# Performance work log

Measured on AMD Instinct MI355X. Metric: run time of the kernel, lower is better.

The kernel has to match this reference:

```python
import jax, jax.numpy as jnp
import numpy as np

N_NODES = 100000
N_EDGES = 1600000
N_CLASS = 10
HIDDEN = 128
BN_EPS = 1e-5


def _bn(h, gamma, beta):
    # BatchNorm1d in training mode: biased batch statistics over the node dim
    m = h.mean(axis=0)
    v = ((h - m) ** 2).mean(axis=0)
    return gamma * (h - m) / jnp.sqrt(v + BN_EPS) + beta


def _mlp(h, w1, b1, g1, t1, w2, b2, g2, t2):
    h = jax.nn.relu(_bn(h @ w1 + b1, g1, t1))
    h = jax.nn.relu(_bn(h @ w2 + b2, g2, t2))
    return h


def _gin_conv(x, edge_index, mlp_params):
    src, dst = edge_index[0], edge_index[1]
    # sum-aggregate neighbor messages: [E, D] gather + scatter-add -> [N, D]
    agg = jax.ops.segment_sum(x[src], dst, num_segments=N_NODES)
    h = x + agg  # (1 + eps) * x + agg, eps = 0
    return _mlp(h, *mlp_params)


def setup_inputs() -> dict:
    key = jax.random.key(0)
    ks = jax.random.split(key, 16)
    x = jax.random.normal(ks[0], (N_NODES, N_CLASS), dtype=jnp.float32)
    edge_index = jax.random.randint(ks[1], (2, N_EDGES), 0, N_NODES, dtype=jnp.int64)
    edge_weight = jax.random.uniform(ks[2], (N_EDGES,), dtype=jnp.float32)

    def lin(k, fan_in, fan_out):
        bound = 1.0 / np.sqrt(fan_in)
        kw, kb = jax.random.split(k)
        w = jax.random.uniform(kw, (fan_in, fan_out), minval=-bound, maxval=bound, dtype=jnp.float32)
        b = jax.random.uniform(kb, (fan_out,), minval=-bound, maxval=bound, dtype=jnp.float32)
        return w, b

    w11, b11 = lin(ks[3], N_CLASS, HIDDEN)
    w12, b12 = lin(ks[4], HIDDEN, HIDDEN)
    w21, b21 = lin(ks[5], HIDDEN, HIDDEN)
    w22, b22 = lin(ks[6], HIDDEN, HIDDEN)
    wf, bf = lin(ks[7], HIDDEN, N_CLASS)
    ones = jnp.ones((HIDDEN,), jnp.float32)
    zeros = jnp.zeros((HIDDEN,), jnp.float32)
    return {
        "x": x, "edge_weight": edge_weight,
        "w11": w11, "b11": b11, "g11": ones, "t11": zeros,
        "w12": w12, "b12": b12, "g12": ones, "t12": zeros,
        "w21": w21, "b21": b21, "g21": ones, "t21": zeros,
        "w22": w22, "b22": b22, "g22": ones, "t22": zeros,
        "wf": wf, "bf": bf,
        "edge_index": edge_index,
    }


def reference(x, edge_weight, w11, b11, g11, t11, w12, b12, g12, t12,
              w21, b21, g21, t21, w22, b22, g22, t22, wf, bf, edge_index):
    h = jax.nn.relu(_gin_conv(x, edge_index, (w11, b11, g11, t11, w12, b12, g12, t12)))
    h = jax.nn.relu(_gin_conv(h, edge_index, (w21, b21, g21, t21, w22, b22, g22, t22)))
    logits = h @ wf + bf
    return jax.nn.log_softmax(logits, axis=1)
```

## Files before the change

### kernel.cpp

```cpp
#include <hip/hip_runtime.h>

#define N_CLASS 10
#define HIDDEN 128
#define BN_EPS 1e-5f

typedef short short8 __attribute__((ext_vector_type(8)));
typedef float floatx4 __attribute__((ext_vector_type(4)));

__device__ __forceinline__ float bf2f(unsigned short u) {
    unsigned int x = ((unsigned int)u) << 16;
    float f; __builtin_memcpy(&f, &x, 4); return f;
}
__device__ __forceinline__ unsigned short f2bf(float f) {
    unsigned int x; __builtin_memcpy(&x, &f, 4);
    x += 0x7FFFu + ((x >> 16) & 1u);
    return (unsigned short)(x >> 16);
}
__device__ __forceinline__ float lo_f(unsigned int u) {
    unsigned int x = u << 16; float f; __builtin_memcpy(&f, &x, 4); return f;
}
__device__ __forceinline__ float hi_f(unsigned int u) {
    unsigned int x = u & 0xffff0000u; float f; __builtin_memcpy(&f, &x, 4); return f;
}


__global__ __launch_bounds__(512) void bhist_k(const int* __restrict__ ei,
                                               int* __restrict__ bhist, int E) {
    __shared__ int h[512];
    int tid = threadIdx.x;
    h[tid] = 0;
    __syncthreads();
    for (int e = blockIdx.x * 512 + tid; e < E; e += gridDim.x * 512)
        atomicAdd(&h[((unsigned)ei[E + e]) >> 8], 1);
    __syncthreads();
    if (h[tid]) atomicAdd(&bhist[tid], h[tid]);
}

__global__ __launch_bounds__(512) void bscan_k(const int* __restrict__ bhist,
                                               int* __restrict__ bstart,
                                               int* __restrict__ bcur, int NBK) {
    __shared__ int sm[512];
    int t = threadIdx.x;
    sm[t] = (t < NBK) ? bhist[t] : 0;
    __syncthreads();
    for (int off = 1; off < 512; off <<= 1) {
        int u = (t >= off) ? sm[t - off] : 0;
        __syncthreads();
        sm[t] += u;
        __syncthreads();
    }
    int excl = (t == 0) ? 0 : sm[t - 1];
    if (t <= NBK) bstart[t] = excl;
    if (t < NBK)  bcur[t]   = excl;
}

__global__ __launch_bounds__(512) void bscatter_k(const int* __restrict__ ei,
                                                  int* __restrict__ bcur,
                                                  unsigned int* __restrict__ pairs, int E) {
    __shared__ int h[512], base[512], cur[512];
    int tid = threadIdx.x;
    h[tid] = 0; cur[tid] = 0;
    __syncthreads();
    int chunk = (E + gridDim.x - 1) / gridDim.x;
    int e0 = blockIdx.x * chunk;
    int e1 = min(e0 + chunk, E);
    for (int e = e0 + tid; e < e1; e += 512)
        atomicAdd(&h[((unsigned)ei[E + e]) >> 8], 1);
    __syncthreads();
    base[tid] = h[tid] ? atomicAdd(&bcur[tid], h[tid]) : 0;
    __syncthreads();
    for (int e = e0 + tid; e < e1; e += 512) {
        unsigned int s = (unsigned int)ei[e];
        unsigned int d = (unsigned int)ei[E + e];
        int bk = d >> 8;
        int r = atomicAdd(&cur[bk], 1);
        pairs[base[bk] + r] = s | ((d & 255u) << 24);
    }
}

__global__ __launch_bounds__(512) void bcsr_k(const unsigned int* __restrict__ pairs,
                                              const int* __restrict__ bstart,
                                              int* __restrict__ row_ptr,
                                              int* __restrict__ cnt,
                                              int* __restrict__ col, int N) {
    __shared__ int h[256], sc[256], cur[256];
    int tid = threadIdx.x;
    if (tid < 256) { h[tid] = 0; cur[tid] = 0; }
    __syncthreads();
    int b = blockIdx.x, lo = b << 8;
    int s = bstart[b], e = bstart[b + 1];
    for (int i = s + tid; i < e; i += 512)
        atomicAdd(&h[pairs[i] >> 24], 1);
    __syncthreads();
    if (tid < 256) sc[tid] = h[tid];
    __syncthreads();
    for (int off = 1; off < 256; off <<= 1) {
        int u = (tid < 256 && tid >= off) ? sc[tid - off] : 0;
        __syncthreads();
        if (tid < 256) sc[tid] += u;
        __syncthreads();
    }
    if (tid < 256) {
        int d = lo + tid;
        if (d < N) { cnt[d] = h[tid]; row_ptr[d] = s + sc[tid] - h[tid]; }
        sc[tid] -= h[tid];
    }
    __syncthreads();
    for (int i = s + tid; i < e; i += 512) {
        unsigned int p = pairs[i];
        int d = p >> 24;
        int r = atomicAdd(&cur[d], 1);
        col[s + sc[d] + r] = (int)(p & 0xFFFFFFu);
    }
}

__global__ void prep_k(const float* __restrict__ W0, const float* __restrict__ W1,
                       const float* __restrict__ W2,
                       unsigned short* __restrict__ T0, unsigned short* __restrict__ T1,
                       unsigned short* __restrict__ T2,
                       float* __restrict__ stats, int* __restrict__ bhist) {
    int y = blockIdx.y;
    int i = blockIdx.x * 256 + threadIdx.x;
    const float* W = (y == 0) ? W0 : (y == 1) ? W1 : W2;
    unsigned short* T = (y == 0) ? T0 : (y == 1) ? T1 : T2;
    if (i < 128 * 128) {
        int k = i >> 7, n = i & 127;
        T[n * 128 + k] = f2bf(W[k * 128 + n]);
    }
    if (y == 0) {
        if (i < 1024) stats[i] = 0.f;
        if (i < 512)  bhist[i] = 0;
    }
}

__global__ void padx_k(const float* __restrict__ X, unsigned short* __restrict__ XP, int N) {
    int i = blockIdx.x * 256 + threadIdx.x;
    if (i >= N * 16) return;
    int node = i >> 4, f = i & 15;
    XP[i] = (f < N_CLASS) ? f2bf(X[node * N_CLASS + f]) : (unsigned short)0;
}

__global__ void gather10_k(const unsigned short* __restrict__ XP, const int* __restrict__ col,
                           const int* __restrict__ rp, const int* __restrict__ cnt,
                           float* __restrict__ out, int N) {
    int t = blockIdx.x * 256 + threadIdx.x;
    int node = t >> 4, f = t & 15;
    if (node >= N) return;
    int start = rp[node], deg = cnt[node];
    float acc = bf2f(XP[node * 16 + f]);
    int j = 0;
    for (; j + 8 <= deg; j += 8) {
        int s0 = col[start + j],     s1 = col[start + j + 1];
        int s2 = col[start + j + 2], s3 = col[start + j + 3];
        int s4 = col[start + j + 4], s5 = col[start + j + 5];
        int s6 = col[start + j + 6], s7 = col[start + j + 7];
        float v0 = bf2f(XP[s0 * 16 + f]);
        float v1 = bf2f(XP[s1 * 16 + f]);
        float v2 = bf2f(XP[s2 * 16 + f]);
        float v3 = bf2f(XP[s3 * 16 + f]);
        float v4 = bf2f(XP[s4 * 16 + f]);
        float v5 = bf2f(XP[s5 * 16 + f]);
        float v6 = bf2f(XP[s6 * 16 + f]);
        float v7 = bf2f(XP[s7 * 16 + f]);
        acc += v0; acc += v1; acc += v2; acc += v3;
        acc += v4; acc += v5; acc += v6; acc += v7;
    }
    for (; j < deg; ++j)
        acc += bf2f(XP[col[start + j] * 16 + f]);
    out[node * 16 + f] = acc;
}

__global__ __launch_bounds__(256) void act2_k(
    const unsigned short* __restrict__ Z, unsigned short* __restrict__ R,
    const float* __restrict__ st, const float* __restrict__ g,
    const float* __restrict__ b, int N, float inv_n) {
    __shared__ float sTab[128], hTab[128];
    int tid = threadIdx.x;
    if (tid < 128) {
        float m = st[tid] * inv_n;
        float v = fmaxf(st[128 + tid] * inv_n - m * m, 0.f);
        float s = g[tid] * rsqrtf(v + BN_EPS);
        sTab[tid] = s;
        hTab[tid] = b[tid] - m * s;
    }
    __syncthreads();
    int total = N * 16;
    for (int i = blockIdx.x * 256 + tid; i < total; i += gridDim.x * 256) {
        int k8 = (i & 15) * 8;
        uint4 v = ((const uint4*)Z)[i];
        unsigned short* us = (unsigned short*)&v;
#pragma unroll
        for (int j = 0; j < 8; ++j) {
            float f = fmaxf(fmaf(bf2f(us[j]), sTab[k8 + j], hTab[k8 + j]), 0.f);
            us[j] = f2bf(f);
        }
        ((uint4*)R)[i] = v;
    }
}

__global__ __launch_bounds__(256) void gather_sum_k(
    const unsigned short* __restrict__ R, const int* __restrict__ col,
    const int* __restrict__ rp, const int* __restrict__ cnt,
    unsigned short* __restrict__ out, int N) {
    int wave = __builtin_amdgcn_readfirstlane((blockIdx.x * 256 + threadIdx.x) >> 6);
    int lane = threadIdx.x & 63;
    if (wave >= N) return;
    int start = __builtin_amdgcn_readfirstlane(rp[wave]);
    int deg   = __builtin_amdgcn_readfirstlane(cnt[wave]);
    const unsigned int* Xv = (const unsigned int*)R;
    unsigned int self = Xv[wave * 64 + lane];
    float a0 = lo_f(self);
    float a1 = hi_f(self);
    int j = 0;
    for (; j + 8 <= deg; j += 8) {
        int n0 = col[start + j],     n1 = col[start + j + 1];
        int n2 = col[start + j + 2], n3 = col[start + j + 3];
        int n4 = col[start + j + 4], n5 = col[start + j + 5];
        int n6 = col[start + j + 6], n7 = col[start + j + 7];
        unsigned int w0 = Xv[n0 * 64 + lane];
        unsigned int w1 = Xv[n1 * 64 + lane];
        unsigned int w2 = Xv[n2 * 64 + lane];
        unsigned int w3 = Xv[n3 * 64 + lane];
        unsigned int w4 = Xv[n4 * 64 + lane];
        unsigned int w5 = Xv[n5 * 64 + lane];
        unsigned int w6 = Xv[n6 * 64 + lane];
        unsigned int w7 = Xv[n7 * 64 + lane];
        a0 += lo_f(w0); a1 += hi_f(w0);
        a0 += lo_f(w1); a1 += hi_f(w1);
        a0 += lo_f(w2); a1 += hi_f(w2);
        a0 += lo_f(w3); a1 += hi_f(w3);
        a0 += lo_f(w4); a1 += hi_f(w4);
        a0 += lo_f(w5); a1 += hi_f(w5);
        a0 += lo_f(w6); a1 += hi_f(w6);
        a0 += lo_f(w7); a1 += hi_f(w7);
    }
    for (; j < deg; ++j) {
        unsigned int v = Xv[col[start + j] * 64 + lane];
        a0 += lo_f(v); a1 += hi_f(v);
    }
    unsigned int o = (unsigned int)f2bf(a0) | ((unsigned int)f2bf(a1) << 16);
    ((unsigned int*)out)[wave * 64 + lane] = o;
}

__global__ __launch_bounds__(128) void gemm10_k(
    const float* __restrict__ A, const float* __restrict__ W,
    const float* __restrict__ bias, unsigned short* __restrict__ C,
    float* __restrict__ stOut, int N) {
    __shared__ float rb[16 * 16];
    const int tid = threadIdx.x;
    float wreg[N_CLASS];
#pragma unroll
    for (int k = 0; k < N_CLASS; ++k) wreg[k] = W[k * HIDDEN + tid];
    float bb = bias[tid];
    float s = 0.f, s2 = 0.f;
    for (int r0 = blockIdx.x * 16; r0 < N; r0 += gridDim.x * 16) {
        int nr = min(16, N - r0);
        for (int i = tid; i < nr * 16; i += 128) rb[i] = A[r0 * 16 + i];
        __syncthreads();
        for (int r = 0; r < nr; ++r) {
            float acc = bb;
#pragma unroll
            for (int k = 0; k < N_CLASS; ++k) acc = fmaf(rb[r * 16 + k], wreg[k], acc);
            C[(r0 + r) * HIDDEN + tid] = f2bf(acc);
            s += acc; s2 += acc * acc;
        }
        __syncthreads();
    }
    atomicAdd(stOut + tid, s);
    atomicAdd(stOut + HIDDEN + tid, s2);
}

template<bool BN>
__global__ __launch_bounds__(256, 3) void gemm_mfma_k(
    const unsigned short* __restrict__ Zin, const unsigned short* __restrict__ Wt,
    const float* __restrict__ bias,
    const float* __restrict__ stIn, const float* __restrict__ gIn,
    const float* __restrict__ tIn,
    unsigned short* __restrict__ Zout, float* __restrict__ stOut,
    int N, float inv_n) {
    __shared__ unsigned short Wl[128 * 136];
    __shared__ unsigned short Al[64 * 136];
    __shared__ float sTab[128], hTab[128], biasTab[128];

    const int tid  = threadIdx.x;
    const int wv   = tid >> 6;
    const int ln   = tid & 63;
    const int half = ln >> 4;
    const int l16  = ln & 15;

    if (tid < 128) {
        biasTab[tid] = bias[tid];
        if (BN) {
            float m = stIn[tid] * inv_n;
            float v = fmaxf(stIn[128 + tid] * inv_n - m * m, 0.f);
            float s = gIn[tid] * rsqrtf(v + BN_EPS);
            sTab[tid] = s;
            hTab[tid] = tIn[tid] - m * s;
        }
    }
    for (int c = tid; c < 2048; c += 256) {
        int n = c >> 4, k8 = c & 15;
        uint4 v = *(const uint4*)(Wt + n * 128 + k8 * 8);
        *(uint4*)(&Wl[n * 136 + k8 * 8]) = v;
    }
    __syncthreads();

    float cs[8], cs2[8];
#pragma unroll
    for (int i = 0; i < 8; ++i) { cs[i] = 0.f; cs2[i] = 0.f; }

    const int ntiles = (N + 63) >> 6;
    for (int tile = blockIdx.x; tile < ntiles; tile += gridDim.x) {
        const int r0 = tile * 64;
        for (int c = tid; c < 1024; c += 256) {
            int r = c >> 4, k8 = c & 15;
            int gr = r0 + r; if (gr >= N) gr = N - 1;
            uint4 v = *(const uint4*)(Zin + gr * 128 + k8 * 8);
            if (BN) {
                unsigned short* us = (unsigned short*)&v;
                int kb = k8 * 8;
#pragma unroll
                for (int j = 0; j < 8; ++j) {
                    float f = fmaxf(fmaf(bf2f(us[j]), sTab[kb + j], hTab[kb + j]), 0.f);
                    us[j] = f2bf(f);
                }
            }
            *(uint4*)(&Al[r * 136 + k8 * 8]) = v;
        }
        __syncthreads();

        short8 afrag[4];
        const int arow = wv * 16 + l16;
#pragma unroll
        for (int s = 0; s < 4; ++s)
            afrag[s] = *(const short8*)(&Al[arow * 136 + s * 32 + half * 8]);
        __syncthreads();

#pragma unroll
        for (int ct = 0; ct < 8; ++ct) {
            floatx4 acc = {0.f, 0.f, 0.f, 0.f};
            const int bn_ = ct * 16 + l16;
#pragma unroll
            for (int s = 0; s < 4; ++s) {
                short8 bfrag = *(const short8*)(&Wl[bn_ * 136 + s * 32 + half * 8]);
                acc = __builtin_amdgcn_mfma_f32_16x16x32_bf16(afrag[s], bfrag, acc, 0, 0, 0);
            }
            float bcol = biasTab[bn_];
#pragma unroll
            for (int r = 0; r < 4; ++r) {
                int lrow = wv * 16 + half * 4 + r;
                float val = acc[r] + bcol;
                if (r0 + lrow < N) { cs[ct] += val; cs2[ct] += val * val; }
                Al[lrow * 136 + bn_] = f2bf(val);
            }
        }
        __syncthreads();

        for (int c = tid; c < 1024; c += 256) {
            int r = c >> 4, k8 = c & 15;
            int gr = r0 + r;
            if (gr < N)
                *(uint4*)(Zout + gr * 128 + k8 * 8) = *(const uint4*)(&Al[r * 136 + k8 * 8]);
        }
        __syncthreads();
    }

    float* red = (float*)Al;
    if (tid < 256) red[tid] = 0.f;
    __syncthreads();
#pragma unroll
    for (int ct = 0; ct < 8; ++ct) {
        float a = cs[ct], b = cs2[ct];
        a += __shfl_xor(a, 16); a += __shfl_xor(a, 32);
        b += __shfl_xor(b, 16); b += __shfl_xor(b, 32);
        if (half == 0) {
            atomicAdd(&red[ct * 16 + l16], a);
            atomicAdd(&red[128 + ct * 16 + l16], b);
        }
    }
    __syncthreads();
    if (tid < 128) {
        atomicAdd(stOut + tid, red[tid]);
        atomicAdd(stOut + 128 + tid, red[128 + tid]);
    }
}

__global__ __launch_bounds__(256) void final_mfma_k(
    const unsigned short* __restrict__ Z, const float* __restrict__ st,
    const float* __restrict__ g, const float* __restrict__ b,
    const float* __restrict__ wf, const float* __restrict__ bfc,
    float* __restrict__ out, int N, float inv_n) {
    __shared__ unsigned short Al[64 * 136];
    __shared__ unsigned short Bl[16 * 136];
    __shared__ float sTab[128], hTab[128], biasTab[16];

    const int tid  = threadIdx.x;
    const int wv   = tid >> 6;
    const int ln   = tid & 63;
    const int half = ln >> 4;
    const int l16  = ln & 15;

    if (tid < 128) {
        float m = st[tid] * inv_n;
        float v = fmaxf(st[128 + tid] * inv_n - m * m, 0.f);
        float s = g[tid] * rsqrtf(v + BN_EPS);
        sTab[tid] = s;
        hTab[tid] = b[tid] - m * s;
    }
    if (tid < 16) biasTab[tid] = (tid < N_CLASS) ? bfc[tid] : -3.0e38f;
    {
        int n = tid >> 4, k8 = (tid & 15) * 8;
        uint4 v;
        unsigned short* us = (unsigned short*)&v;
#pragma unroll
        for (int j = 0; j < 8; ++j)
            us[j] = (n < N_CLASS) ? f2bf(wf[(k8 + j) * N_CLASS + n]) : (unsigned short)0;
        *(uint4*)(&Bl[n * 136 + k8]) = v;
    }
    __syncthreads();

    short8 bfrag[4];
#pragma unroll
    for (int s = 0; s < 4; ++s)
        bfrag[s] = *(const short8*)(&Bl[l16 * 136 + s * 32 + half * 8]);

    const int ntiles = (N + 63) >> 6;
    for (int tile = blockIdx.x; tile < ntiles; tile += gridDim.x) {
        const int r0 = tile * 64;
        for (int c = tid; c < 1024; c += 256) {
            int r = c >> 4, k8 = c & 15;
            int gr = r0 + r; if (gr >= N) gr = N - 1;
            uint4 v = *(const uint4*)(Z + gr * 128 + k8 * 8);
            unsigned short* us = (unsigned short*)&v;
            int kb = k8 * 8;
#pragma unroll
            for (int j = 0; j < 8; ++j) {
                float f = fmaxf(fmaf(bf2f(us[j]), sTab[kb + j], hTab[kb + j]), 0.f);
                us[j] = f2bf(f);
            }
            *(uint4*)(&Al[r * 136 + k8 * 8]) = v;
        }
        __syncthreads();

        short8 afrag[4];
        const int arow = wv * 16 + l16;
#pragma unroll
        for (int s = 0; s < 4; ++s)
            afrag[s] = *(const short8*)(&Al[arow * 136 + s * 32 + half * 8]);
        __syncthreads();

        floatx4 acc = {0.f, 0.f, 0.f, 0.f};
#pragma unroll
        for (int s = 0; s < 4; ++s)
            acc = __builtin_amdgcn_mfma_f32_16x16x32_bf16(afrag[s], bfrag[s], acc, 0, 0, 0);

        float bcol = biasTab[l16];
#pragma unroll
        for (int r = 0; r < 4; ++r) {
            float lg = acc[r] + bcol;
            float mx = lg;
            mx = fmaxf(mx, __shfl_xor(mx, 1));
            mx = fmaxf(mx, __shfl_xor(mx, 2));
            mx = fmaxf(mx, __shfl_xor(mx, 4));
            mx = fmaxf(mx, __shfl_xor(mx, 8));
            float p = __expf(lg - mx);
            float se = p;
            se += __shfl_xor(se, 1);
            se += __shfl_xor(se, 2);
            se += __shfl_xor(se, 4);
            se += __shfl_xor(se, 8);
            float ls = __logf(se);
            int grow = r0 + wv * 16 + half * 4 + r;
            if (l16 < N_CLASS && grow < N)
                out[grow * N_CLASS + l16] = lg - mx - ls;
        }
    }
}


extern "C" void kernel_launch(void* const* d_in, const int* in_sizes, int n_in,
                              void* d_out, int out_size, void* d_ws, size_t ws_size,
                              hipStream_t stream) {
    const float* x   = (const float*)d_in[0];
    const float* w11 = (const float*)d_in[2];
    const float* b11 = (const float*)d_in[3];
    const float* g11 = (const float*)d_in[4];
    const float* t11 = (const float*)d_in[5];
    const float* w12 = (const float*)d_in[6];
    const float* b12 = (const float*)d_in[7];
    const float* g12 = (const float*)d_in[8];
    const float* t12 = (const float*)d_in[9];
    const float* w21 = (const float*)d_in[10];
    const float* b21 = (const float*)d_in[11];
    const float* g21 = (const float*)d_in[12];
    const float* t21 = (const float*)d_in[13];
    const float* w22 = (const float*)d_in[14];
    const float* b22 = (const float*)d_in[15];
    const float* g22 = (const float*)d_in[16];
    const float* t22 = (const float*)d_in[17];
    const float* wf  = (const float*)d_in[18];
    const float* bf  = (const float*)d_in[19];
    const int*   ei  = (const int*)d_in[20];

    const int N = in_sizes[0] / N_CLASS;
    const int E = in_sizes[1];
    const float inv_n = 1.0f / (float)N;
    const int NBK = (N + 255) >> 8;

    char* base = (char*)d_ws;
    size_t off = 0;
    auto take = [&](size_t bytes) { void* p = base + off; off += (bytes + 15) & ~(size_t)15; return p; };
    float*          stats   = (float*)take(1024 * 4);
    unsigned short* xp      = (unsigned short*)take((size_t)N * 16 * 2);
    float*          h0      = (float*)take((size_t)N * 16 * 4);
    int*            cnt     = (int*)take((size_t)N * 4);
    int*            row_ptr = (int*)take((size_t)N * 4);
    int*            bhist   = (int*)take(512 * 4);
    int*            bstart  = (int*)take(520 * 4);
    int*            bcur    = (int*)take(512 * 4);
    unsigned int*   pairs   = (unsigned int*)take((size_t)E * 4);
    int*            col     = (int*)take((size_t)E * 4);
    unsigned short* bufA    = (unsigned short*)take((size_t)N * HIDDEN * 2);
    unsigned short* bufB    = (unsigned short*)take((size_t)N * HIDDEN * 2);
    unsigned short* bufC    = (unsigned short*)take((size_t)N * HIDDEN * 2);
    unsigned short* Wt1     = (unsigned short*)take(128 * 128 * 2);
    unsigned short* Wt2     = (unsigned short*)take(128 * 128 * 2);
    unsigned short* Wt3     = (unsigned short*)take(128 * 128 * 2);

    prep_k<<<dim3(64, 3), 256, 0, stream>>>(w12, w21, w22, Wt1, Wt2, Wt3,
                                            stats, bhist);
    padx_k<<<(N * 16 + 255) / 256, 256, 0, stream>>>(x, xp, N);

    bhist_k<<<256, 512, 0, stream>>>(ei, bhist, E);
    bscan_k<<<1, 512, 0, stream>>>(bhist, bstart, bcur, NBK);
    bscatter_k<<<256, 512, 0, stream>>>(ei, bcur, pairs, E);
    bcsr_k<<<NBK, 512, 0, stream>>>(pairs, bstart, row_ptr, cnt, col, N);

    gather10_k<<<(N * 16 + 255) / 256, 256, 0, stream>>>(xp, col, row_ptr, cnt, h0, N);
    gemm10_k<<<512, 128, 0, stream>>>(h0, w11, b11, bufA, stats, N);
    gemm_mfma_k<true><<<768, 256, 0, stream>>>(bufA, Wt1, b12, stats, g11, t11,
                                               bufB, stats + 256, N, inv_n);

    act2_k<<<3125, 256, 0, stream>>>(bufB, bufC, stats + 256, g12, t12, N, inv_n);
    gather_sum_k<<<(N * 64 + 255) / 256, 256, 0, stream>>>(bufC, col, row_ptr, cnt,
                                                           bufA, N);

    gemm_mfma_k<false><<<768, 256, 0, stream>>>(bufA, Wt2, b21, nullptr, nullptr, nullptr,
                                                bufB, stats + 512, N, inv_n);
    gemm_mfma_k<true><<<768, 256, 0, stream>>>(bufB, Wt3, b22, stats + 512, g21, t21,
                                               bufA, stats + 768, N, inv_n);

    final_mfma_k<<<782, 256, 0, stream>>>(bufA, stats + 768, g22, t22,
                                          wf, bf, (float*)d_out, N, inv_n);
}
```

Measured before the change: 404.7 us.

## Precompute per-block bucket offsets via two-level scan; unroll gather by sixteen

The bucket sort now records a per-block histogram in bhist_k. A new bscan2_k kernel prefix-scans those counts into deterministic per-block base offsets, so bscatter_k no longer recounts its destination histogram or takes global atomic offsets. This removes one full pass over the destination indices and the atomic contention on bcur, at the cost of an extra small kernel launch and a 512x256 offset table. The hidden-layer gather loop also gets a 16-wide unrolled stage to keep more independent loads in flight per wave, which raises register pressure.

```diff
diff --git a/kernel.cpp b/kernel.cpp
--- a/kernel.cpp
+++ b/kernel.cpp
@@ -25,41 +25,11 @@
 
 
 __global__ __launch_bounds__(512) void bhist_k(const int* __restrict__ ei,
-                                               int* __restrict__ bhist, int E) {
+                                               int* __restrict__ bhist,
+                                               int* __restrict__ bbase, int E) {
     __shared__ int h[512];
     int tid = threadIdx.x;
     h[tid] = 0;
-    __syncthreads();
-    for (int e = blockIdx.x * 512 + tid; e < E; e += gridDim.x * 512)
-        atomicAdd(&h[((unsigned)ei[E + e]) >> 8], 1);
-    __syncthreads();
-    if (h[tid]) atomicAdd(&bhist[tid], h[tid]);
-}
-
-__global__ __launch_bounds__(512) void bscan_k(const int* __restrict__ bhist,
-                                               int* __restrict__ bstart,
-                                               int* __restrict__ bcur, int NBK) {
-    __shared__ int sm[512];
-    int t = threadIdx.x;
-    sm[t] = (t < NBK) ? bhist[t] : 0;
-    __syncthreads();
-    for (int off = 1; off < 512; off <<= 1) {
-        int u = (t >= off) ? sm[t - off] : 0;
-        __syncthreads();
-        sm[t] += u;
-        __syncthreads();
-    }
-    int excl = (t == 0) ? 0 : sm[t - 1];
-    if (t <= NBK) bstart[t] = excl;
-    if (t < NBK)  bcur[t]   = excl;
-}
-
-__global__ __launch_bounds__(512) void bscatter_k(const int* __restrict__ ei,
-                                                  int* __restrict__ bcur,
-                                                  unsigned int* __restrict__ pairs, int E) {
-    __shared__ int h[512], base[512], cur[512];
-    int tid = threadIdx.x;
-    h[tid] = 0; cur[tid] = 0;
     __syncthreads();
     int chunk = (E + gridDim.x - 1) / gridDim.x;
     int e0 = blockIdx.x * chunk;
@@ -67,8 +37,54 @@
     for (int e = e0 + tid; e < e1; e += 512)
         atomicAdd(&h[((unsigned)ei[E + e]) >> 8], 1);
     __syncthreads();
-    base[tid] = h[tid] ? atomicAdd(&bcur[tid], h[tid]) : 0;
-    __syncthreads();
+    bbase[tid * 256 + blockIdx.x] = h[tid];
+    if (h[tid]) atomicAdd(&bhist[tid], h[tid]);
+}
+
+__global__ __launch_bounds__(512) void bscan_k(const int* __restrict__ bhist,
+                                               int* __restrict__ bstart, int NBK) {
+    __shared__ int sm[512];
+    int t = threadIdx.x;
+    sm[t] = (t < NBK) ? bhist[t] : 0;
+    __syncthreads();
+    for (int off = 1; off < 512; off <<= 1) {
+        int u = (t >= off) ? sm[t - off] : 0;
+        __syncthreads();
+        sm[t] += u;
+        __syncthreads();
+    }
+    bstart[t] = (t == 0) ? 0 : sm[t - 1];
+    if (t == 0) bstart[512] = sm[511];
+}
+
+__global__ __launch_bounds__(256) void bscan2_k(int* __restrict__ bbase,
+                                                const int* __restrict__ bstart) {
+    __shared__ int sm[256];
+    int b = blockIdx.x;
+    int t = threadIdx.x;
+    int v = bbase[b * 256 + t];
+    sm[t] = v;
+    __syncthreads();
+    for (int off = 1; off < 256; off <<= 1) {
+        int u = (t >= off) ? sm[t - off] : 0;
+        __syncthreads();
+        sm[t] += u;
+        __syncthreads();
+    }
+    bbase[b * 256 + t] = bstart[b] + sm[t] - v;
+}
+
+__global__ __launch_bounds__(512) void bscatter_k(const int* __restrict__ ei,
+                                                  const int* __restrict__ bbase,
+                                                  unsigned int* __restrict__ pairs, int E) {
+    __shared__ int base[512], cur[512];
+    int tid = threadIdx.x;
+    base[tid] = bbase[tid * 256 + blockIdx.x];
+    cur[tid] = 0;
+    __syncthreads();
+    int chunk = (E + gridDim.x - 1) / gridDim.x;
+    int e0 = blockIdx.x * chunk;
+    int e1 = min(e0 + chunk, E);
     for (int e = e0 + tid; e < e1; e += 512) {
         unsigned int s = (unsigned int)ei[e];
         unsigned int d = (unsigned int)ei[E + e];
@@ -212,6 +228,48 @@
     float a0 = lo_f(self);
     float a1 = hi_f(self);
     int j = 0;
+    for (; j + 16 <= deg; j += 16) {
+        int n0  = col[start + j],      n1  = col[start + j + 1];
+        int n2  = col[start + j + 2],  n3  = col[start + j + 3];
+        int n4  = col[start + j + 4],  n5  = col[start + j + 5];
+        int n6  = col[start + j + 6],  n7  = col[start + j + 7];
+        int n8  = col[start + j + 8],  n9  = col[start + j + 9];
+        int n10 = col[start + j + 10], n11 = col[start + j + 11];
+        int n12 = col[start + j + 12], n13 = col[start + j + 13];
+        int n14 = col[start + j + 14], n15 = col[start + j + 15];
+        unsigned int w0  = Xv[n0  * 64 + lane];
+        unsigned int w1  = Xv[n1  * 64 + lane];
+        unsigned int w2  = Xv[n2  * 64 + lane];
+        unsigned int w3  = Xv[n3  * 64 + lane];
+        unsigned int w4  = Xv[n4  * 64 + lane];
+        unsigned int w5  = Xv[n5  * 64 + lane];
+        unsigned int w6  = Xv[n6  * 64 + lane];
+        unsigned int w7  = Xv[n7  * 64 + lane];
+        unsigned int w8  = Xv[n8  * 64 + lane];
+        unsigned int w9  = Xv[n9  * 64 + lane];
+        unsigned int w10 = Xv[n10 * 64 + lane];
+        unsigned int w11 = Xv[n11 * 64 + lane];
+        unsigned int w12 = Xv[n12 * 64 + lane];
+        unsigned int w13 = Xv[n13 * 64 + lane];
+        unsigned int w14 = Xv[n14 * 64 + lane];
+        unsigned int w15 = Xv[n15 * 64 + lane];
+        a0 += lo_f(w0);  a1 += hi_f(w0);
+        a0 += lo_f(w1);  a1 += hi_f(w1);
+        a0 += lo_f(w2);  a1 += hi_f(w2);
+        a0 += lo_f(w3);  a1 += hi_f(w3);
+        a0 += lo_f(w4);  a1 += hi_f(w4);
+        a0 += lo_f(w5);  a1 += hi_f(w5);
+        a0 += lo_f(w6);  a1 += hi_f(w6);
+        a0 += lo_f(w7);  a1 += hi_f(w7);
+        a0 += lo_f(w8);  a1 += hi_f(w8);
+        a0 += lo_f(w9);  a1 += hi_f(w9);
+        a0 += lo_f(w10); a1 += hi_f(w10);
+        a0 += lo_f(w11); a1 += hi_f(w11);
+        a0 += lo_f(w12); a1 += hi_f(w12);
+        a0 += lo_f(w13); a1 += hi_f(w13);
+        a0 += lo_f(w14); a1 += hi_f(w14);
+        a0 += lo_f(w15); a1 += hi_f(w15);
+    }
     for (; j + 8 <= deg; j += 8) {
         int n0 = col[start + j],     n1 = col[start + j + 1];
         int n2 = col[start + j + 2], n3 = col[start + j + 3];
@@ -517,7 +575,7 @@
     int*            row_ptr = (int*)take((size_t)N * 4);
     int*            bhist   = (int*)take(512 * 4);
     int*            bstart  = (int*)take(520 * 4);
-    int*            bcur    = (int*)take(512 * 4);
+    int*            bbase   = (int*)take(512 * 256 * 4);
     unsigned int*   pairs   = (unsigned int*)take((size_t)E * 4);
     int*            col     = (int*)take((size_t)E * 4);
     unsigned short* bufA    = (unsigned short*)take((size_t)N * HIDDEN * 2);
@@ -531,9 +589,10 @@
                                             stats, bhist);
     padx_k<<<(N * 16 + 255) / 256, 256, 0, stream>>>(x, xp, N);
 
-    bhist_k<<<256, 512, 0, stream>>>(ei, bhist, E);
-    bscan_k<<<1, 512, 0, stream>>>(bhist, bstart, bcur, NBK);
-    bscatter_k<<<256, 512, 0, stream>>>(ei, bcur, pairs, E);
+    bhist_k<<<256, 512, 0, stream>>>(ei, bhist, bbase, E);
+    bscan_k<<<1, 512, 0, stream>>>(bhist, bstart, NBK);
+    bscan2_k<<<NBK, 256, 0, stream>>>(bbase, bstart);
+    bscatter_k<<<256, 512, 0, stream>>>(ei, bbase, pairs, E);
     bcsr_k<<<NBK, 512, 0, stream>>>(pairs, bstart, row_ptr, cnt, col, N);
 
     gather10_k<<<(N * 16 + 255) / 256, 256, 0, stream>>>(xp, col, row_ptr, cnt, h0, N);
```

Result: no change. 400.9 us (-0.9%).
